# Kernel tuning notes

Measured on AMD Instinct MI355X. Metric: run time of the kernel, lower is better.

## Reference

```python
import jax, jax.numpy as jnp
import numpy as np

EPS_NORM = 1e-12
BN_EPS = 1e-5

def rmsnorm(x, gamma):
    # F.normalize(x, dim=-1) * gamma * dim**0.5
    n = jnp.maximum(jnp.linalg.norm(x, axis=-1, keepdims=True), EPS_NORM)
    return x / n * gamma * np.float32(np.sqrt(x.shape[-1]))

def conv1d(x, w, pad):
    # x: (B,C,T), w: (O,I,K)
    return jax.lax.conv_general_dilated(x, w, (1,), [(pad, pad)],
                                        dimension_numbers=('NCH', 'OIH', 'NCH'))

def maxpool3(x):
    # kernel 3, stride 1, pad 1 over last axis
    return jax.lax.reduce_window(x, -jnp.inf, jax.lax.max,
                                 (1, 1, 3), (1, 1, 1), [(0, 0), (0, 0), (1, 1)])

def gelu(x):
    return jax.nn.gelu(x, approximate=False)  # matches torch F.gelu default


def setup_inputs() -> dict:
    key = jax.random.key(0)
    ks = jax.random.split(key, 16)
    B, N, D, E, H, NF = 4, 4096, 512, 4, 1024, 32
    s = 0.02
    inp = {
        'x': jax.random.normal(ks[0], (B, N, D), jnp.float32),
        'left_k': 2048,
        'gamma1': jnp.ones((D,), jnp.float32),
        'gamma2': jnp.ones((D,), jnp.float32),
        'attn_w': jax.random.normal(ks[1], (D, 1), jnp.float32) * s,
        'attn_b': jnp.zeros((1,), jnp.float32),
        'gate_w': jax.random.normal(ks[2], (D, E), jnp.float32) * s,
        'expert_w1': jax.random.normal(ks[3], (E, D, H), jnp.float32) * s,
        'expert_w2': jax.random.normal(ks[4], (E, H, D), jnp.float32) * s,
        'bott_w': jax.random.normal(ks[5], (NF, D, 1), jnp.float32) * s,
        'conv_w39': jax.random.normal(ks[6], (NF, NF, 39), jnp.float32) * s,
        'conv_w19': jax.random.normal(ks[7], (NF, NF, 19), jnp.float32) * s,
        'conv_w9': jax.random.normal(ks[8], (NF, NF, 9), jnp.float32) * s,
        'mp_w': jax.random.normal(ks[9], (NF, D, 1), jnp.float32) * s,
        'bn_g': jnp.ones((NF * 4,), jnp.float32),
        'bn_b': jnp.zeros((NF * 4,), jnp.float32),
        'proj_w': jax.random.normal(ks[10], (NF * 4, D), jnp.float32) * s,
        'proj_b': jnp.zeros((D,), jnp.float32),
    }
    return inp


def reference(x, left_k, gamma1, gamma2, attn_w, attn_b, gate_w,
              expert_w1, expert_w2, bott_w, conv_w39, conv_w19, conv_w9,
              mp_w, bn_g, bn_b, proj_w, proj_b):
    B, N, D = x.shape
    E = gate_w.shape[-1]

    x_n = rmsnorm(x, gamma1)
    scores = jax.nn.sigmoid(x_n @ attn_w + attn_b)            # (B,N,1)
    xs = x_n * scores                                          # (B,N,D)

    # top-k token selection (remain_ratio < 1 path)
    _, top_idx = jax.lax.top_k(scores[..., 0], left_k)         # (B,left_k)
    sorted_idx = jnp.sort(top_idx, axis=1)
    left_x = jnp.take_along_axis(xs, sorted_idx[..., None], axis=1)
    # complement sum via scatter mask (faithful to scatter_/gather/sum)
    sel = jnp.zeros((B, N), x.dtype).at[jnp.arange(B)[:, None], sorted_idx].set(1.0)
    extra = jnp.einsum('bn,bnd->bd', 1.0 - sel, xs)[:, None, :]
    xcat = jnp.concatenate([left_x, extra], axis=1)            # (B,left_k+1,D)

    x_n2 = rmsnorm(xcat, gamma2)

    # dense soft MoE
    gate = jax.nn.softmax(x_n2 @ gate_w, axis=-1)              # (B,T,E)
    h = gelu(jnp.einsum('btd,edh->bteh', x_n2, expert_w1))
    eo = jnp.einsum('bteh,ehd->bted', h, expert_w2)
    moe_out = jnp.einsum('bte,bted->btd', gate, eo)
    moe_loss = E * jnp.sum(jnp.mean(gate, axis=(0, 1)) ** 2)

    # Inception branch (channels-first)
    xc = jnp.transpose(x_n2, (0, 2, 1))                        # (B,D,T)
    xb = conv1d(xc, bott_w, 0)                                 # (B,32,T)
    outs = [conv1d(xb, conv_w39, 19), conv1d(xb, conv_w19, 9),
            conv1d(xb, conv_w9, 4), conv1d(maxpool3(xc), mp_w, 0)]
    cat = jnp.concatenate(outs, axis=1)                        # (B,128,T)
    mu = jnp.mean(cat, axis=(0, 2), keepdims=True)
    var = jnp.var(cat, axis=(0, 2), keepdims=True)
    bn = (cat - mu) / jnp.sqrt(var + BN_EPS) * bn_g[None, :, None] + bn_b[None, :, None]
    incep = gelu(bn)
    incep_out = jnp.transpose(incep, (0, 2, 1)) @ proj_w + proj_b  # (B,T,D)

    out = xcat + moe_out + incep_out
    return gelu(out), moe_loss
```

## Files before the change

### kernel.cpp

```cpp
#include <hip/hip_runtime.h>
#include <hip/hip_bf16.h>
#include <math.h>

#define DEV __device__ __forceinline__

constexpr int B_ = 4, N_ = 4096, D_ = 512, E_ = 4, H_ = 1024, NF_ = 32;
constexpr int KL_ = 2048, T_ = KL_ + 1;
constexpr int TOK_ = B_ * T_;
constexpr int SP_ = 2304;

typedef __bf16 bf16x8 __attribute__((ext_vector_type(8)));
typedef float f32x4 __attribute__((ext_vector_type(4)));

DEV float gelu_f(float x){
  float t = __expf(-1.702f * x);
  return x * __builtin_amdgcn_rcpf(1.0f + t);
}
DEV float bf2f(unsigned short u){ union{unsigned int i; float f;} c; c.i = (unsigned)u << 16; return c.f; }
DEV unsigned pack2(float a, float b){
  __hip_bfloat16 ha = __float2bfloat16(a), hb = __float2bfloat16(b);
  unsigned short ua = *(unsigned short*)&ha, ub = *(unsigned short*)&hb;
  return (unsigned)ua | ((unsigned)ub << 16);
}

DEV float wave_sum(float v){
  #pragma unroll
  for (int off = 32; off > 0; off >>= 1) v += __shfl_down(v, off, 64);
  return v;
}

DEV float block_sum256(float v, float* sm){
  v = wave_sum(v);
  int lane = threadIdx.x & 63, wid = threadIdx.x >> 6;
  if (lane == 0) sm[wid] = v;
  __syncthreads();
  if (threadIdx.x == 0) sm[0] = sm[0] + sm[1] + sm[2] + sm[3];
  __syncthreads();
  float r = sm[0];
  __syncthreads();
  return r;
}

__global__ void k_rms_score(const float* __restrict__ x, const float* __restrict__ g,
                            const float* __restrict__ aw, const float* __restrict__ ab,
                            float* __restrict__ scores, float* __restrict__ scale){
  __shared__ float sm[4];
  int row = blockIdx.x; int tid = threadIdx.x;
  const float* xr = x + (size_t)row * D_;
  float v0 = xr[tid], v1 = xr[tid + 256];
  float ss = block_sum256(v0 * v0 + v1 * v1, sm);
  float a  = block_sum256(v0 * g[tid] * aw[tid] + v1 * g[tid + 256] * aw[tid + 256], sm);
  float n = fmaxf(sqrtf(ss), 1e-12f);
  float inv = 22.627416997969522f / n;
  float z = inv * a + ab[0];
  float s = 1.0f / (1.0f + expf(-z));
  if (tid == 0){ scores[row] = s; scale[row] = inv * s; }
}

__global__ void k_select(const float* __restrict__ scores, int* __restrict__ flags){
  __shared__ float s[N_];
  __shared__ int cnts[4][64];
  int b = blockIdx.y; int tid = threadIdx.x;
  int tile = blockIdx.x * 64;
  const float4* src = (const float4*)(scores + (size_t)b * N_);
  for (int j = tid; j < N_ / 4; j += 256) ((float4*)s)[j] = src[j];
  __syncthreads();
  int tok = tid & 63, part = tid >> 6;
  int i = tile + tok;
  float si = s[i];
  int cnt = 0;
  const float4* sp = (const float4*)(s + part * 1024);
  int jb = part * 1024;
  #pragma unroll 4
  for (int j = 0; j < 256; j++){
    float4 v = sp[j];
    int j4 = jb + j * 4;
    cnt += (v.x > si) || (v.x == si && (j4 + 0) < i);
    cnt += (v.y > si) || (v.y == si && (j4 + 1) < i);
    cnt += (v.z > si) || (v.z == si && (j4 + 2) < i);
    cnt += (v.w > si) || (v.w == si && (j4 + 3) < i);
  }
  cnts[part][tok] = cnt;
  __syncthreads();
  if (tid < 64){
    int c = cnts[0][tid] + cnts[1][tid] + cnts[2][tid] + cnts[3][tid];
    flags[(size_t)b * N_ + tile + tid] = (c < KL_) ? 1 : 0;
  }
}

__global__ void k_compact(const int* __restrict__ flags, int* __restrict__ idx){
  __shared__ int wsum[4];
  int b = blockIdx.x; int tid = threadIdx.x;
  const int* fb = flags + (size_t)b * N_;
  int f[16]; int cnt = 0;
  #pragma unroll
  for (int i = 0; i < 16; i++){ f[i] = fb[tid * 16 + i]; cnt += f[i]; }
  int lane = tid & 63, wid = tid >> 6;
  int v = cnt;
  #pragma unroll
  for (int off = 1; off < 64; off <<= 1){
    int t = __shfl_up(v, off, 64);
    if (lane >= off) v += t;
  }
  if (lane == 63) wsum[wid] = v;
  __syncthreads();
  int base = v - cnt;
  for (int w = 0; w < wid; w++) base += wsum[w];
  int* ib = idx + (size_t)b * KL_;
  #pragma unroll
  for (int i = 0; i < 16; i++){
    if (f[i]) ib[base++] = tid * 16 + i;
  }
}

__global__ void k_gather(const float* __restrict__ x, const float* __restrict__ scale,
                         const float* __restrict__ g1, const int* __restrict__ idx,
                         float* __restrict__ xcat){
  size_t i = (size_t)blockIdx.x * 256 + threadIdx.x;
  int d = (int)(i & 511);
  int p = (int)((i >> 9) & (KL_ - 1));
  int b = (int)(i >> 20);
  int tok = idx[(size_t)b * KL_ + p];
  float sc = scale[(size_t)b * N_ + tok];
  xcat[((size_t)b * T_ + p) * D_ + d] = x[((size_t)b * N_ + tok) * D_ + d] * sc * g1[d];
}

__global__ void k_extra1(const float* __restrict__ x, const float* __restrict__ scale,
                         const int* __restrict__ flags, float* __restrict__ part){
  int b = blockIdx.y, blk = blockIdx.x;
  int tid = threadIdx.x;
  const int* fb = flags + (size_t)b * N_ + blk * 64;
  const float* sb = scale + (size_t)b * N_ + blk * 64;
  const float2* xp = (const float2*)(x + ((size_t)b * N_ + blk * 64) * D_) + tid;
  float2 acc = {0.f, 0.f};
  for (int i = 0; i < 64; i++){
    if (!fb[i]){
      float s = sb[i];
      float2 v = xp[(size_t)i * 256];
      acc.x += v.x * s; acc.y += v.y * s;
    }
  }
  float* pr = part + ((size_t)(b * 64 + blk)) * D_;
  pr[tid * 2] = acc.x; pr[tid * 2 + 1] = acc.y;
}

__global__ void k_extra2(const float* __restrict__ part, const float* __restrict__ g1,
                         float* __restrict__ xcat){
  int b = blockIdx.y; int d = blockIdx.x * 256 + threadIdx.x;
  float s = 0.f;
  for (int i = 0; i < 64; i++) s += part[((size_t)(b * 64 + i)) * D_ + d];
  xcat[((size_t)b * T_ + KL_) * D_ + d] = s * g1[d];
}

__global__ void k_rms2gate(const float* __restrict__ xc, const float* __restrict__ g,
                           const float* __restrict__ gw,
                           __hip_bfloat16* __restrict__ xn2b, float* __restrict__ gate){
  __shared__ float sm[4];
  __shared__ float sg[16];
  int row = blockIdx.x; int tid = threadIdx.x;
  const float* xr = xc + (size_t)row * D_;
  float v0 = xr[tid], v1 = xr[tid + 256];
  float ss = block_sum256(v0 * v0 + v1 * v1, sm);
  float n = fmaxf(sqrtf(ss), 1e-12f);
  float inv = 22.627416997969522f / n;
  float xn0 = v0 * inv * g[tid], xn1 = v1 * inv * g[tid + 256];
  __hip_bfloat16* ob = xn2b + (size_t)row * D_;
  ob[tid] = __float2bfloat16(xn0); ob[tid + 256] = __float2bfloat16(xn1);
  const float4* gw4 = (const float4*)gw;
  float4 wa = gw4[tid], wb = gw4[tid + 256];
  float l0 = xn0 * wa.x + xn1 * wb.x, l1 = xn0 * wa.y + xn1 * wb.y;
  float l2 = xn0 * wa.z + xn1 * wb.z, l3 = xn0 * wa.w + xn1 * wb.w;
  l0 = wave_sum(l0); l1 = wave_sum(l1); l2 = wave_sum(l2); l3 = wave_sum(l3);
  int lane = tid & 63, wid = tid >> 6;
  if (lane == 0){ sg[wid*4+0]=l0; sg[wid*4+1]=l1; sg[wid*4+2]=l2; sg[wid*4+3]=l3; }
  __syncthreads();
  if (tid == 0){
    float a0 = sg[0]+sg[4]+sg[8]+sg[12];
    float a1 = sg[1]+sg[5]+sg[9]+sg[13];
    float a2 = sg[2]+sg[6]+sg[10]+sg[14];
    float a3 = sg[3]+sg[7]+sg[11]+sg[15];
    float m = fmaxf(fmaxf(a0, a1), fmaxf(a2, a3));
    float e0 = expf(a0-m), e1 = expf(a1-m), e2 = expf(a2-m), e3 = expf(a3-m);
    float is = 1.f / (e0+e1+e2+e3);
    float* gr = gate + (size_t)row * 4;
    gr[0]=e0*is; gr[1]=e1*is; gr[2]=e2*is; gr[3]=e3*is;
  }
}

__global__ void k_gsumloss(const float* __restrict__ gate, float* __restrict__ o){
  __shared__ float sm[16];
  int tid = threadIdx.x;
  float4 a = {0.f, 0.f, 0.f, 0.f};
  for (int r = tid; r < TOK_; r += 256){
    float4 v = *(const float4*)(gate + (size_t)r * 4);
    a.x += v.x; a.y += v.y; a.z += v.z; a.w += v.w;
  }
  a.x = wave_sum(a.x); a.y = wave_sum(a.y); a.z = wave_sum(a.z); a.w = wave_sum(a.w);
  int lane = tid & 63, wid = tid >> 6;
  if (lane == 0){ sm[wid*4]=a.x; sm[wid*4+1]=a.y; sm[wid*4+2]=a.z; sm[wid*4+3]=a.w; }
  __syncthreads();
  if (tid == 0){
    float l = 0.f;
    #pragma unroll
    for (int e = 0; e < 4; e++){
      float s = sm[e] + sm[4+e] + sm[8+e] + sm[12+e];
      float m = s / (float)TOK_;
      l += m * m;
    }
    o[0] = (float)E_ * l;
  }
}

__global__ void k_trb(const float* __restrict__ in, __hip_bfloat16* __restrict__ out,
                      int R, int C){
  __shared__ float t[32][33];
  int mat = blockIdx.z;
  in  += (size_t)mat * R * C;
  out += (size_t)mat * R * C;
  int c0 = blockIdx.x * 32, r0 = blockIdx.y * 32;
  int j = threadIdx.x & 31, i4 = threadIdx.x >> 5;
  #pragma unroll
  for (int k = 0; k < 4; k++){
    int i = i4 * 4 + k;
    t[i][j] = in[(size_t)(r0 + i) * C + c0 + j];
  }
  __syncthreads();
  #pragma unroll
  for (int k = 0; k < 4; k++){
    int i = i4 * 4 + k;
    out[(size_t)(c0 + i) * R + r0 + j] = __float2bfloat16(t[j][i]);
  }
}

__global__ void k_trb2(const float* __restrict__ in, __hip_bfloat16* __restrict__ out){
  __shared__ float t[32][33];
  int e = blockIdx.z;
  const float* ip = in + (size_t)e * H_ * D_;
  __hip_bfloat16* op = out + (size_t)e * H_;
  int c0 = blockIdx.x * 32, r0 = blockIdx.y * 32;
  int j = threadIdx.x & 31, i4 = threadIdx.x >> 5;
  #pragma unroll
  for (int k = 0; k < 4; k++){
    int i = i4 * 4 + k;
    t[i][j] = ip[(size_t)(r0 + i) * D_ + c0 + j];
  }
  __syncthreads();
  #pragma unroll
  for (int k = 0; k < 4; k++){
    int i = i4 * 4 + k;
    int v = r0 + j;
    int pv = (v & ~63) | ((v & 15) << 2) | ((v >> 4) & 3);
    op[(size_t)(c0 + i) * 4096 + pv] = __float2bfloat16(t[j][i]);
  }
}

__global__ void k_wpack(const float* __restrict__ w39, const float* __restrict__ w19,
                        const float* __restrict__ w9, __hip_bfloat16* __restrict__ wcb){
  int i = blockIdx.x * 256 + threadIdx.x;
  if (i >= 73728) return;
  const float* w; int KP, KW, base;
  if (i < 40960){ w = w39; KP = 40; KW = 39; base = 0; }
  else if (i < 61440){ w = w19; KP = 20; KW = 19; base = 40960; }
  else { w = w9; KP = 12; KW = 9; base = 61440; }
  int li = i - base;
  int oc = li / (32 * KP);
  int rem = li % (32 * KP);
  int k = rem >> 5, ic = rem & 31;
  float v = (k < KW) ? w[((size_t)oc * 32 + ic) * KW + k] : 0.f;
  wcb[i] = __float2bfloat16(v);
}

template<int EPI>
__launch_bounds__(512)
__global__ void gemm_bt(const __hip_bfloat16* __restrict__ A,
                        const __hip_bfloat16* __restrict__ Bt,
                        __hip_bfloat16* __restrict__ Cb, size_t zstride,
                        int M, int N, int K, int kloc,
                        const float* __restrict__ gatep){
  __shared__ __align__(16) char smem[2][24576];
  int tid = threadIdx.x;
  unsigned gx = gridDim.x;
  unsigned nwg = gx * gridDim.y;
  unsigned orig = blockIdx.x + gx * blockIdx.y;
  unsigned q = nwg >> 3, r = nwg & 7;
  unsigned xcd = orig & 7, loc = orig >> 3;
  unsigned wg = (xcd < r ? xcd * (q + 1) : r * (q + 1) + (xcd - r) * q) + loc;
  int m0 = (int)(wg / gx) * 256, n0 = (int)(wg % gx) * 128;
  int z = blockIdx.z;
  int koff = z * kloc;
  int ln = tid & 63, wid = tid >> 6;
  int wm = wid >> 1, wn = wid & 1;

  f32x4 acc[4][4] = {};

  auto stage = [&](int buf, int k0){
    #pragma unroll
    for (int c = 0; c < 2; c++){
      int ii = tid + c * 512;
      int rr = ii >> 2, s = ii & 3;
      int gm = m0 + rr; gm = gm < M ? gm : M - 1;
      const __hip_bfloat16* gp = A + (size_t)gm * K + (koff + k0 + ((s ^ (rr & 3)) << 3));
      __builtin_amdgcn_global_load_lds(
          (const __attribute__((address_space(1))) void*)gp,
          (__attribute__((address_space(3))) void*)&smem[buf][ii * 16], 16, 0, 0);
    }
    {
      int ii = tid;
      int rr = ii >> 2, s = ii & 3;
      const __hip_bfloat16* gp = Bt + (size_t)(n0 + rr) * K + (koff + k0 + ((s ^ (rr & 3)) << 3));
      __builtin_amdgcn_global_load_lds(
          (const __attribute__((address_space(1))) void*)gp,
          (__attribute__((address_space(3))) void*)&smem[buf][16384 + ii * 16], 16, 0, 0);
    }
  };

  int nk = kloc >> 5;
  stage(0, 0);
  __syncthreads();
  int slotb = (((ln >> 4) ^ (ln & 3)) << 4);
  for (int t = 0; t < nk; t++){
    int buf = t & 1;
    if (t + 1 < nk) stage(buf ^ 1, (t + 1) << 5);
    bf16x8 af[4], bfr[4];
    #pragma unroll
    for (int m = 0; m < 4; m++){
      int R = wm * 64 + m * 16 + (ln & 15);
      af[m] = *(const bf16x8*)&smem[buf][R * 64 + slotb];
    }
    #pragma unroll
    for (int n = 0; n < 4; n++){
      int R = wn * 64 + n * 16 + (ln & 15);
      bfr[n] = *(const bf16x8*)&smem[buf][16384 + R * 64 + slotb];
    }
    #pragma unroll
    for (int m = 0; m < 4; m++)
      #pragma unroll
      for (int n = 0; n < 4; n++)
        acc[m][n] = __builtin_amdgcn_mfma_f32_16x16x32_bf16(af[m], bfr[n], acc[m][n], 0, 0, 0);
    __syncthreads();
  }

  __hip_bfloat16* Co = Cb + (size_t)z * zstride;
  int e = n0 >> 10;
  int lr = ln & 15;
  #pragma unroll
  for (int m = 0; m < 4; m++){
    int rb = m0 + wm * 64 + m * 16 + ((ln >> 4) << 2);
    float gv[4];
    if (EPI == 1){
      #pragma unroll
      for (int r2 = 0; r2 < 4; r2++)
        gv[r2] = (rb + r2 < M) ? gatep[(size_t)(rb + r2) * 4 + e] : 0.f;
    }
    #pragma unroll
    for (int r2 = 0; r2 < 4; r2++){
      int row = rb + r2;
      if (row < M){
        float v0 = acc[m][0][r2], v1 = acc[m][1][r2];
        float v2 = acc[m][2][r2], v3 = acc[m][3][r2];
        if (EPI == 1){
          v0 = gelu_f(v0) * gv[r2]; v1 = gelu_f(v1) * gv[r2];
          v2 = gelu_f(v2) * gv[r2]; v3 = gelu_f(v3) * gv[r2];
        }
        uint2 pk; pk.x = pack2(v0, v1); pk.y = pack2(v2, v3);
        size_t ci = (size_t)row * N + (n0 + wn * 64 + 4 * lr);
        *(uint2*)&Co[ci] = pk;
      }
    }
  }
}

__global__ void k_1x1F(const __hip_bfloat16* __restrict__ xn2b, const float* __restrict__ bw,
                       const float* __restrict__ mw,
                       __hip_bfloat16* __restrict__ xbp, float* __restrict__ cat){
  __shared__ float Xs[32 * 33];
  __shared__ float Ws[32 * 36];
  int type = blockIdx.y;
  const float* w = type == 0 ? bw : mw;
  int tid = threadIdx.x;
  int G0 = blockIdx.x * 32;
  int tok = tid & 31, grp = tid >> 5;
  float acc[4] = {};
  for (int d0 = 0; d0 < D_; d0 += 32){
    {
      int tt = tid >> 3, dc = (tid & 7) * 4;
      int g = G0 + tt;
      float4 v = {0.f, 0.f, 0.f, 0.f};
      if (g < TOK_){
        const __hip_bfloat16* p = xn2b + (size_t)g * D_ + d0 + dc;
        ushort4 rw = *(const ushort4*)p;
        v.x = bf2f(rw.x); v.y = bf2f(rw.y); v.z = bf2f(rw.z); v.w = bf2f(rw.w);
        if (type == 1){
          int t = g % T_;
          if (t > 0){
            ushort4 u = *(const ushort4*)(p - D_);
            v.x = fmaxf(v.x, bf2f(u.x)); v.y = fmaxf(v.y, bf2f(u.y));
            v.z = fmaxf(v.z, bf2f(u.z)); v.w = fmaxf(v.w, bf2f(u.w));
          }
          if (t < T_ - 1){
            ushort4 u = *(const ushort4*)(p + D_);
            v.x = fmaxf(v.x, bf2f(u.x)); v.y = fmaxf(v.y, bf2f(u.y));
            v.z = fmaxf(v.z, bf2f(u.z)); v.w = fmaxf(v.w, bf2f(u.w));
          }
        }
      }
      float* xd = &Xs[tt * 33 + dc];
      xd[0] = v.x; xd[1] = v.y; xd[2] = v.z; xd[3] = v.w;
    }
    for (int j = tid; j < 1024; j += 256){
      int f = j >> 5, d = j & 31;
      Ws[d * 36 + f] = w[(size_t)f * D_ + d0 + d];
    }
    __syncthreads();
    const float* xr = &Xs[tok * 33];
    #pragma unroll 8
    for (int d = 0; d < 32; d++){
      float xv = xr[d];
      const float4* w4 = (const float4*)&Ws[d * 36 + grp * 4];
      float4 a = w4[0];
      acc[0] += xv * a.x; acc[1] += xv * a.y; acc[2] += xv * a.z; acc[3] += xv * a.w;
    }
    __syncthreads();
  }
  int g = G0 + tok;
  if (g < TOK_){
    if (type == 0){
      int bb = g / T_, t = g % T_;
      __hip_bfloat16* op = xbp + ((size_t)(bb * SP_ + 32 + t)) * 32 + grp * 4;
      #pragma unroll
      for (int j = 0; j < 4; j++) op[j] = __float2bfloat16(acc[j]);
    } else {
      float* op = cat + (size_t)g * 128 + 96 + grp * 4;
      #pragma unroll
      for (int j = 0; j < 4; j++) op[j] = acc[j];
    }
  }
}

template<int KP, int PAD, int OFF, int TYPE>
DEV void convm_body(const __hip_bfloat16* __restrict__ xbp,
                    const __hip_bfloat16* __restrict__ wcb,
                    float* __restrict__ cat, char* smem){
  constexpr int R = KP * 32;
  int t0 = blockIdx.x * 128, b = blockIdx.y;
  int tid = threadIdx.x;
  for (int j = tid; j < 768; j += 256){
    int r = j >> 2, c = j & 3;
    int rg = b * SP_ + 32 + t0 - PAD + r;
    const __hip_bfloat16* gp = xbp + (size_t)rg * 32 + ((c ^ (r & 3)) << 3);
    __builtin_amdgcn_global_load_lds(
        (const __attribute__((address_space(1))) void*)gp,
        (__attribute__((address_space(3))) void*)(smem + j * 16), 16, 0, 0);
  }
  __syncthreads();
  int ln = tid & 63, wid = tid >> 6;
  int lr = ln & 15, lg = ln >> 4;
  int tb = wid * 32;
  const __hip_bfloat16* wt = wcb + OFF;
  const __hip_bfloat16* bp0 = wt + (size_t)lr * R + lg * 8;
  const __hip_bfloat16* bp1 = wt + (size_t)(16 + lr) * R + lg * 8;
  f32x4 acc[2][2] = {};
  bf16x8 bc0 = *(const bf16x8*)bp0;
  bf16x8 bc1 = *(const bf16x8*)bp1;
  #pragma unroll 4
  for (int s = 0; s < KP; s++){
    bf16x8 bn0 = bc0, bn1 = bc1;
    if (s + 1 < KP){
      bn0 = *(const bf16x8*)(bp0 + (s + 1) * 32);
      bn1 = *(const bf16x8*)(bp1 + (s + 1) * 32);
    }
    int ra0 = tb + lr + s;
    int ra1 = tb + 16 + lr + s;
    bf16x8 a0 = *(const bf16x8*)(smem + ra0 * 64 + ((lg ^ (ra0 & 3)) << 4));
    bf16x8 a1 = *(const bf16x8*)(smem + ra1 * 64 + ((lg ^ (ra1 & 3)) << 4));
    acc[0][0] = __builtin_amdgcn_mfma_f32_16x16x32_bf16(a0, bc0, acc[0][0], 0, 0, 0);
    acc[0][1] = __builtin_amdgcn_mfma_f32_16x16x32_bf16(a0, bc1, acc[0][1], 0, 0, 0);
    acc[1][0] = __builtin_amdgcn_mfma_f32_16x16x32_bf16(a1, bc0, acc[1][0], 0, 0, 0);
    acc[1][1] = __builtin_amdgcn_mfma_f32_16x16x32_bf16(a1, bc1, acc[1][1], 0, 0, 0);
    bc0 = bn0; bc1 = bn1;
  }
  #pragma unroll
  for (int m = 0; m < 2; m++){
    int rb = tb + m * 16 + ((ln >> 4) << 2);
    #pragma unroll
    for (int n = 0; n < 2; n++){
      int oc = n * 16 + lr;
      #pragma unroll
      for (int j2 = 0; j2 < 4; j2++){
        int tp = t0 + rb + j2;
        if (tp < T_)
          cat[((size_t)b * T_ + tp) * 128 + TYPE * 32 + oc] = acc[m][n][j2];
      }
    }
  }
}

__global__ __launch_bounds__(256)
void k_convM(const __hip_bfloat16* __restrict__ xbp,
             const __hip_bfloat16* __restrict__ wcb, float* __restrict__ cat){
  __shared__ __align__(16) char smem[192 * 64];
  if (blockIdx.z == 0)      convm_body<40, 19, 0,     0>(xbp, wcb, cat, smem);
  else if (blockIdx.z == 1) convm_body<20, 9,  40960, 1>(xbp, wcb, cat, smem);
  else                      convm_body<12, 4,  61440, 2>(xbp, wcb, cat, smem);
}

__global__ void k_bnstat(const float* __restrict__ cat, float* __restrict__ stats){
  __shared__ float sm[512];
  int tid = threadIdx.x;
  float s = 0.f, q = 0.f;
  for (int rp = blockIdx.x; rp < TOK_ / 2; rp += gridDim.x){
    float v = cat[(size_t)rp * 256 + tid];
    s += v; q += v * v;
  }
  sm[tid] = s; sm[256 + tid] = q;
  __syncthreads();
  if (tid < 128){
    atomicAdd(&stats[tid], sm[tid] + sm[tid + 128]);
    atomicAdd(&stats[128 + tid], sm[256 + tid] + sm[256 + tid + 128]);
  }
}

__global__ void k_bnact(const float* __restrict__ cat, __hip_bfloat16* __restrict__ catb,
                        const float* __restrict__ stats,
                        const float* __restrict__ g, const float* __restrict__ b){
  int i = blockIdx.x * 256 + threadIdx.x;
  int c = i & 127;
  float mu = stats[c] * (1.f / TOK_);
  float var = stats[128 + c] * (1.f / TOK_) - mu * mu;
  float v = cat[i];
  v = (v - mu) * rsqrtf(var + 1e-5f) * g[c] + b[c];
  catb[i] = __float2bfloat16(gelu_f(v));
}

__global__ void k_final(const float* __restrict__ xcat, const __hip_bfloat16* __restrict__ moeb,
                        size_t zs, const __hip_bfloat16* __restrict__ ioutb,
                        const float* __restrict__ pb, float* __restrict__ out){
  size_t i = ((size_t)blockIdx.x * 256 + threadIdx.x) * 2;
  int p = (int)(i & 511);
  size_t rowbase = i - p;
  float s0 = 0.f, s1 = 0.f;
  #pragma unroll
  for (int z = 0; z < 4; z++){
    unsigned u = *(const unsigned*)&moeb[(size_t)z * zs + i];
    s0 += bf2f((unsigned short)(u & 0xffff));
    s1 += bf2f((unsigned short)(u >> 16));
  }
  unsigned v = *(const unsigned*)&ioutb[i];
  s0 += bf2f((unsigned short)(v & 0xffff));
  s1 += bf2f((unsigned short)(v >> 16));
  int d0 = (p & ~63) | ((p & 3) << 4) | ((p >> 2) & 15);
  int p1 = p + 1;
  int d1 = (p1 & ~63) | ((p1 & 3) << 4) | ((p1 >> 2) & 15);
  s0 += xcat[rowbase + d0] + pb[d0];
  s1 += xcat[rowbase + d1] + pb[d1];
  out[rowbase + d0] = gelu_f(s0);
  out[rowbase + d1] = gelu_f(s1);
}

extern "C" void kernel_launch(void* const* d_in, const int* in_sizes, int n_in,
                              void* d_out, int out_size, void* d_ws, size_t ws_size,
                              hipStream_t stream){
  const float* x      = (const float*)d_in[0];
  const float* gamma1 = (const float*)d_in[2];
  const float* gamma2 = (const float*)d_in[3];
  const float* attn_w = (const float*)d_in[4];
  const float* attn_b = (const float*)d_in[5];
  const float* gate_w = (const float*)d_in[6];
  const float* ew1    = (const float*)d_in[7];
  const float* ew2    = (const float*)d_in[8];
  const float* bott_w = (const float*)d_in[9];
  const float* w39    = (const float*)d_in[10];
  const float* w19    = (const float*)d_in[11];
  const float* w9     = (const float*)d_in[12];
  const float* mp_w   = (const float*)d_in[13];
  const float* bn_g   = (const float*)d_in[14];
  const float* bn_b   = (const float*)d_in[15];
  const float* proj_w = (const float*)d_in[16];
  const float* proj_b = (const float*)d_in[17];
  float* out = (float*)d_out;

  float* ws = (float*)d_ws;
  size_t off = 0;
  auto alloc = [&](size_t n){ size_t o = off; off += (n + 63) & ~(size_t)63; return o; };
  size_t f_hb   = alloc((size_t)TOK_ * 4096 / 2);
  size_t f_sc   = alloc(B_ * N_);
  size_t f_sca  = alloc(B_ * N_);
  size_t f_fl   = alloc(B_ * N_);
  size_t f_idx  = alloc(B_ * KL_);
  size_t f_xcat = alloc((size_t)TOK_ * D_);
  size_t f_moeb = alloc((size_t)4 * TOK_ * D_ / 2 + 64);
  size_t f_gate = alloc(TOK_ * E_);
  size_t f_st   = alloc(256);
  size_t f_xbp  = alloc((size_t)B_ * SP_ * 32 / 2);
  size_t f_cat  = alloc((size_t)TOK_ * 128);
  size_t f_wb   = alloc((size_t)(E_ * D_ * H_) + (size_t)TOK_ * D_ / 2 + 64);
  size_t f_part = alloc((size_t)B_ * 64 * D_);
  size_t f_wcb  = alloc(73728 / 2 + 64);
  size_t f_pjb  = alloc(512 * 128 / 2 + 64);
  (void)ws_size; (void)in_sizes; (void)n_in; (void)out_size;

  float* sc   = ws + f_sc;
  float* sca  = ws + f_sca;
  int*   fl   = (int*)(ws + f_fl);
  int*   idx  = (int*)(ws + f_idx);
  float* xcat = ws + f_xcat;
  float* gate = ws + f_gate;
  float* stats= ws + f_st;
  float* cat  = ws + f_cat;
  float* part = ws + f_part;
  __hip_bfloat16* moeb  = (__hip_bfloat16*)(ws + f_moeb);
  __hip_bfloat16* xbp   = (__hip_bfloat16*)(ws + f_xbp);
  __hip_bfloat16* wcb   = (__hip_bfloat16*)(ws + f_wcb);
  __hip_bfloat16* projb = (__hip_bfloat16*)(ws + f_pjb);
  __hip_bfloat16* hbuf  = (__hip_bfloat16*)(ws + f_hb);
  __hip_bfloat16* ioutb = (__hip_bfloat16*)(ws + f_hb);
  __hip_bfloat16* catb  = (__hip_bfloat16*)(ws + f_hb + 4196416);
  __hip_bfloat16* w1b  = (__hip_bfloat16*)(ws + f_wb);
  __hip_bfloat16* w2b  = w1b + (size_t)E_ * D_ * H_;
  __hip_bfloat16* xn2b = w2b + (size_t)E_ * D_ * H_;

  hipMemsetAsync(stats, 0, 256 * sizeof(float), stream);
  hipMemsetAsync(xbp, 0, (size_t)B_ * SP_ * 32 * sizeof(__hip_bfloat16), stream);

  k_trb<<<dim3(H_/32, D_/32, E_), 256, 0, stream>>>(ew1, w1b, D_, H_);
  k_trb2<<<dim3(D_/32, H_/32, E_), 256, 0, stream>>>(ew2, w2b);
  k_trb<<<dim3(D_/32, 128/32, 1), 256, 0, stream>>>(proj_w, projb, 128, D_);
  k_wpack<<<288, 256, 0, stream>>>(w39, w19, w9, wcb);

  k_rms_score<<<B_ * N_, 256, 0, stream>>>(x, gamma1, attn_w, attn_b, sc, sca);
  k_select<<<dim3(N_ / 64, B_), 256, 0, stream>>>(sc, fl);
  k_compact<<<B_, 256, 0, stream>>>(fl, idx);
  k_gather<<<(B_ * KL_ * D_) / 256, 256, 0, stream>>>(x, sca, gamma1, idx, xcat);
  k_extra1<<<dim3(64, B_), 256, 0, stream>>>(x, sca, fl, part);
  k_extra2<<<dim3(2, B_), 256, 0, stream>>>(part, gamma1, xcat);
  k_rms2gate<<<TOK_, 256, 0, stream>>>(xcat, gamma2, gate_w, xn2b, gate);
  k_gsumloss<<<1, 256, 0, stream>>>(gate, out + (size_t)TOK_ * D_);

  int mt = (TOK_ + 255) / 256;
  size_t zs = (size_t)TOK_ * D_;
  gemm_bt<1><<<dim3(4096/128, mt), 512, 0, stream>>>(
      xn2b, w1b, hbuf, 0, TOK_, 4096, D_, D_, gate);
  gemm_bt<0><<<dim3(D_/128, mt, 4), 512, 0, stream>>>(
      hbuf, w2b, moeb, zs, TOK_, D_, 4096, 1024, nullptr);

  int t32 = (TOK_ + 31) / 32;
  k_1x1F<<<dim3(t32, 2), 256, 0, stream>>>(xn2b, bott_w, mp_w, xbp, cat);
  k_convM<<<dim3(17, 4, 3), 256, 0, stream>>>(xbp, wcb, cat);
  k_bnstat<<<256, 256, 0, stream>>>(cat, stats);
  k_bnact<<<(TOK_ * 128) / 256, 256, 0, stream>>>(cat, catb, stats, bn_g, bn_b);
  gemm_bt<0><<<dim3(D_/128, mt), 512, 0, stream>>>(
      catb, projb, ioutb, 0, TOK_, D_, 128, 128, nullptr);
  k_final<<<((size_t)TOK_ * D_) / 512, 256, 0, stream>>>(xcat, moeb, zs, ioutb, proj_b, out);
}
```

Measured before the change: 313.7 us.

## Fuse gather with RMSNorm/gate, fold BN stats into convs, merge weight prep

Merges the gather and extra-token kernels with the second RMSNorm and gate softmax, so xcat is produced and normalized in one pass and stored as bf16 instead of fp32. Batch-norm sum and sum-of-squares are accumulated with atomics in the 1x1 and conv epilogues, which removes the separate k_bnstat pass over cat. The four weight transpose and pack kernels and the stats memset are merged into one launch. The bf16 xcat residual in the final sum loses some precision, and the float atomics make the BN statistics depend on summation order.

```diff
diff --git a/kernel.cpp b/kernel.cpp
--- a/kernel.cpp
+++ b/kernel.cpp
@@ -113,16 +113,57 @@
   }
 }
 
-__global__ void k_gather(const float* __restrict__ x, const float* __restrict__ scale,
-                         const float* __restrict__ g1, const int* __restrict__ idx,
-                         float* __restrict__ xcat){
-  size_t i = (size_t)blockIdx.x * 256 + threadIdx.x;
-  int d = (int)(i & 511);
-  int p = (int)((i >> 9) & (KL_ - 1));
-  int b = (int)(i >> 20);
+DEV void rms2_tail(int row, float xc0, float xc1,
+                   const float* __restrict__ g2, const float* __restrict__ gw,
+                   __hip_bfloat16* __restrict__ xcatb,
+                   __hip_bfloat16* __restrict__ xn2b, float* __restrict__ gate,
+                   float* sm, float* sg){
+  int tid = threadIdx.x;
+  __hip_bfloat16* xb = xcatb + (size_t)row * D_;
+  xb[tid] = __float2bfloat16(xc0); xb[tid + 256] = __float2bfloat16(xc1);
+  float ss = block_sum256(xc0 * xc0 + xc1 * xc1, sm);
+  float n = fmaxf(sqrtf(ss), 1e-12f);
+  float inv = 22.627416997969522f / n;
+  float xn0 = xc0 * inv * g2[tid], xn1 = xc1 * inv * g2[tid + 256];
+  __hip_bfloat16* ob = xn2b + (size_t)row * D_;
+  ob[tid] = __float2bfloat16(xn0); ob[tid + 256] = __float2bfloat16(xn1);
+  const float4* gw4 = (const float4*)gw;
+  float4 wa = gw4[tid], wb = gw4[tid + 256];
+  float l0 = xn0 * wa.x + xn1 * wb.x, l1 = xn0 * wa.y + xn1 * wb.y;
+  float l2 = xn0 * wa.z + xn1 * wb.z, l3 = xn0 * wa.w + xn1 * wb.w;
+  l0 = wave_sum(l0); l1 = wave_sum(l1); l2 = wave_sum(l2); l3 = wave_sum(l3);
+  int lane = tid & 63, wid = tid >> 6;
+  if (lane == 0){ sg[wid*4+0]=l0; sg[wid*4+1]=l1; sg[wid*4+2]=l2; sg[wid*4+3]=l3; }
+  __syncthreads();
+  if (tid == 0){
+    float a0 = sg[0]+sg[4]+sg[8]+sg[12];
+    float a1 = sg[1]+sg[5]+sg[9]+sg[13];
+    float a2 = sg[2]+sg[6]+sg[10]+sg[14];
+    float a3 = sg[3]+sg[7]+sg[11]+sg[15];
+    float m = fmaxf(fmaxf(a0, a1), fmaxf(a2, a3));
+    float e0 = expf(a0-m), e1 = expf(a1-m), e2 = expf(a2-m), e3 = expf(a3-m);
+    float is = 1.f / (e0+e1+e2+e3);
+    float* gr = gate + (size_t)row * 4;
+    gr[0]=e0*is; gr[1]=e1*is; gr[2]=e2*is; gr[3]=e3*is;
+  }
+}
+
+__global__ void k_gatherrms(const float* __restrict__ x, const float* __restrict__ scale,
+                            const float* __restrict__ g1, const float* __restrict__ g2,
+                            const float* __restrict__ gw, const int* __restrict__ idx,
+                            __hip_bfloat16* __restrict__ xcatb,
+                            __hip_bfloat16* __restrict__ xn2b, float* __restrict__ gate){
+  __shared__ float sm[4];
+  __shared__ float sg[16];
+  int rid = blockIdx.x;
+  int b = rid >> 11, p = rid & (KL_ - 1);
+  int tid = threadIdx.x;
   int tok = idx[(size_t)b * KL_ + p];
   float sc = scale[(size_t)b * N_ + tok];
-  xcat[((size_t)b * T_ + p) * D_ + d] = x[((size_t)b * N_ + tok) * D_ + d] * sc * g1[d];
+  const float* xr = x + ((size_t)b * N_ + tok) * D_;
+  float xc0 = xr[tid] * sc * g1[tid];
+  float xc1 = xr[tid + 256] * sc * g1[tid + 256];
+  rms2_tail(b * T_ + p, xc0, xc1, g2, gw, xcatb, xn2b, gate, sm, sg);
 }
 
 __global__ void k_extra1(const float* __restrict__ x, const float* __restrict__ scale,
@@ -144,47 +185,20 @@
   pr[tid * 2] = acc.x; pr[tid * 2 + 1] = acc.y;
 }
 
-__global__ void k_extra2(const float* __restrict__ part, const float* __restrict__ g1,
-                         float* __restrict__ xcat){
-  int b = blockIdx.y; int d = blockIdx.x * 256 + threadIdx.x;
-  float s = 0.f;
-  for (int i = 0; i < 64; i++) s += part[((size_t)(b * 64 + i)) * D_ + d];
-  xcat[((size_t)b * T_ + KL_) * D_ + d] = s * g1[d];
-}
-
-__global__ void k_rms2gate(const float* __restrict__ xc, const float* __restrict__ g,
-                           const float* __restrict__ gw,
-                           __hip_bfloat16* __restrict__ xn2b, float* __restrict__ gate){
+__global__ void k_extra2r(const float* __restrict__ part, const float* __restrict__ g1,
+                          const float* __restrict__ g2, const float* __restrict__ gw,
+                          __hip_bfloat16* __restrict__ xcatb,
+                          __hip_bfloat16* __restrict__ xn2b, float* __restrict__ gate){
   __shared__ float sm[4];
   __shared__ float sg[16];
-  int row = blockIdx.x; int tid = threadIdx.x;
-  const float* xr = xc + (size_t)row * D_;
-  float v0 = xr[tid], v1 = xr[tid + 256];
-  float ss = block_sum256(v0 * v0 + v1 * v1, sm);
-  float n = fmaxf(sqrtf(ss), 1e-12f);
-  float inv = 22.627416997969522f / n;
-  float xn0 = v0 * inv * g[tid], xn1 = v1 * inv * g[tid + 256];
-  __hip_bfloat16* ob = xn2b + (size_t)row * D_;
-  ob[tid] = __float2bfloat16(xn0); ob[tid + 256] = __float2bfloat16(xn1);
-  const float4* gw4 = (const float4*)gw;
-  float4 wa = gw4[tid], wb = gw4[tid + 256];
-  float l0 = xn0 * wa.x + xn1 * wb.x, l1 = xn0 * wa.y + xn1 * wb.y;
-  float l2 = xn0 * wa.z + xn1 * wb.z, l3 = xn0 * wa.w + xn1 * wb.w;
-  l0 = wave_sum(l0); l1 = wave_sum(l1); l2 = wave_sum(l2); l3 = wave_sum(l3);
-  int lane = tid & 63, wid = tid >> 6;
-  if (lane == 0){ sg[wid*4+0]=l0; sg[wid*4+1]=l1; sg[wid*4+2]=l2; sg[wid*4+3]=l3; }
-  __syncthreads();
-  if (tid == 0){
-    float a0 = sg[0]+sg[4]+sg[8]+sg[12];
-    float a1 = sg[1]+sg[5]+sg[9]+sg[13];
-    float a2 = sg[2]+sg[6]+sg[10]+sg[14];
-    float a3 = sg[3]+sg[7]+sg[11]+sg[15];
-    float m = fmaxf(fmaxf(a0, a1), fmaxf(a2, a3));
-    float e0 = expf(a0-m), e1 = expf(a1-m), e2 = expf(a2-m), e3 = expf(a3-m);
-    float is = 1.f / (e0+e1+e2+e3);
-    float* gr = gate + (size_t)row * 4;
-    gr[0]=e0*is; gr[1]=e1*is; gr[2]=e2*is; gr[3]=e3*is;
-  }
+  int b = blockIdx.x; int tid = threadIdx.x;
+  float s0 = 0.f, s1 = 0.f;
+  for (int i = 0; i < 64; i++){
+    const float* pr = part + ((size_t)(b * 64 + i)) * D_;
+    s0 += pr[tid]; s1 += pr[tid + 256];
+  }
+  float xc0 = s0 * g1[tid], xc1 = s1 * g1[tid + 256];
+  rms2_tail(b * T_ + KL_, xc0, xc1, g2, gw, xcatb, xn2b, gate, sm, sg);
 }
 
 __global__ void k_gsumloss(const float* __restrict__ gate, float* __restrict__ o){
@@ -211,13 +225,10 @@
   }
 }
 
-__global__ void k_trb(const float* __restrict__ in, __hip_bfloat16* __restrict__ out,
-                      int R, int C){
+DEV void trb_tile(const float* __restrict__ in, __hip_bfloat16* __restrict__ out,
+                  int R, int C, int bx, int by){
   __shared__ float t[32][33];
-  int mat = blockIdx.z;
-  in  += (size_t)mat * R * C;
-  out += (size_t)mat * R * C;
-  int c0 = blockIdx.x * 32, r0 = blockIdx.y * 32;
+  int c0 = bx * 32, r0 = by * 32;
   int j = threadIdx.x & 31, i4 = threadIdx.x >> 5;
   #pragma unroll
   for (int k = 0; k < 4; k++){
@@ -232,42 +243,61 @@
   }
 }
 
-__global__ void k_trb2(const float* __restrict__ in, __hip_bfloat16* __restrict__ out){
-  __shared__ float t[32][33];
-  int e = blockIdx.z;
-  const float* ip = in + (size_t)e * H_ * D_;
-  __hip_bfloat16* op = out + (size_t)e * H_;
-  int c0 = blockIdx.x * 32, r0 = blockIdx.y * 32;
-  int j = threadIdx.x & 31, i4 = threadIdx.x >> 5;
-  #pragma unroll
-  for (int k = 0; k < 4; k++){
-    int i = i4 * 4 + k;
-    t[i][j] = ip[(size_t)(r0 + i) * D_ + c0 + j];
-  }
-  __syncthreads();
-  #pragma unroll
-  for (int k = 0; k < 4; k++){
-    int i = i4 * 4 + k;
-    int v = r0 + j;
-    int pv = (v & ~63) | ((v & 15) << 2) | ((v >> 4) & 3);
-    op[(size_t)(c0 + i) * 4096 + pv] = __float2bfloat16(t[j][i]);
-  }
-}
-
-__global__ void k_wpack(const float* __restrict__ w39, const float* __restrict__ w19,
-                        const float* __restrict__ w9, __hip_bfloat16* __restrict__ wcb){
-  int i = blockIdx.x * 256 + threadIdx.x;
-  if (i >= 73728) return;
-  const float* w; int KP, KW, base;
-  if (i < 40960){ w = w39; KP = 40; KW = 39; base = 0; }
-  else if (i < 61440){ w = w19; KP = 20; KW = 19; base = 40960; }
-  else { w = w9; KP = 12; KW = 9; base = 61440; }
-  int li = i - base;
-  int oc = li / (32 * KP);
-  int rem = li % (32 * KP);
-  int k = rem >> 5, ic = rem & 31;
-  float v = (k < KW) ? w[((size_t)oc * 32 + ic) * KW + k] : 0.f;
-  wcb[i] = __float2bfloat16(v);
+__global__ void k_wprep(const float* __restrict__ ew1, const float* __restrict__ ew2,
+                        const float* __restrict__ proj_w,
+                        const float* __restrict__ w39, const float* __restrict__ w19,
+                        const float* __restrict__ w9,
+                        __hip_bfloat16* __restrict__ w1b, __hip_bfloat16* __restrict__ w2b,
+                        __hip_bfloat16* __restrict__ projb, __hip_bfloat16* __restrict__ wcb,
+                        float* __restrict__ stats){
+  int blk = blockIdx.x;
+  int tid = threadIdx.x;
+  if (blk < 2048){
+    int e = blk >> 9, rem = blk & 511;
+    int by = rem >> 5, bx = rem & 31;
+    trb_tile(ew1 + (size_t)e * D_ * H_, w1b + (size_t)e * D_ * H_, D_, H_, bx, by);
+  } else if (blk < 4096){
+    int r = blk - 2048;
+    int e = r >> 9, r2 = r & 511;
+    int bx = r2 & 15, by = r2 >> 4;
+    __shared__ float t[32][33];
+    const float* ip = ew2 + (size_t)e * H_ * D_;
+    __hip_bfloat16* op = w2b + (size_t)e * H_;
+    int c0 = bx * 32, r0 = by * 32;
+    int j = tid & 31, i4 = tid >> 5;
+    #pragma unroll
+    for (int k = 0; k < 4; k++){
+      int i = i4 * 4 + k;
+      t[i][j] = ip[(size_t)(r0 + i) * D_ + c0 + j];
+    }
+    __syncthreads();
+    #pragma unroll
+    for (int k = 0; k < 4; k++){
+      int i = i4 * 4 + k;
+      int v = r0 + j;
+      int pv = (v & ~63) | ((v & 15) << 2) | ((v >> 4) & 3);
+      op[(size_t)(c0 + i) * 4096 + pv] = __float2bfloat16(t[j][i]);
+    }
+  } else if (blk < 4160){
+    int r = blk - 4096;
+    trb_tile(proj_w, projb, 128, D_, r & 15, r >> 4);
+  } else if (blk < 4448){
+    int i = (blk - 4160) * 256 + tid;
+    if (i < 73728){
+      const float* w; int KP, KW, base;
+      if (i < 40960){ w = w39; KP = 40; KW = 39; base = 0; }
+      else if (i < 61440){ w = w19; KP = 20; KW = 19; base = 40960; }
+      else { w = w9; KP = 12; KW = 9; base = 61440; }
+      int li = i - base;
+      int oc = li / (32 * KP);
+      int rem = li % (32 * KP);
+      int k = rem >> 5, ic = rem & 31;
+      float v = (k < KW) ? w[((size_t)oc * 32 + ic) * KW + k] : 0.f;
+      wcb[i] = __float2bfloat16(v);
+    }
+  } else {
+    stats[tid] = 0.f;
+  }
 }
 
 template<int EPI>
@@ -372,7 +402,8 @@
 
 __global__ void k_1x1F(const __hip_bfloat16* __restrict__ xn2b, const float* __restrict__ bw,
                        const float* __restrict__ mw,
-                       __hip_bfloat16* __restrict__ xbp, float* __restrict__ cat){
+                       __hip_bfloat16* __restrict__ xbp, float* __restrict__ cat,
+                       float* __restrict__ stats){
   __shared__ float Xs[32 * 33];
   __shared__ float Ws[32 * 36];
   int type = blockIdx.y;
@@ -423,7 +454,8 @@
     __syncthreads();
   }
   int g = G0 + tok;
-  if (g < TOK_){
+  bool valid = g < TOK_;
+  if (valid){
     if (type == 0){
       int bb = g / T_, t = g % T_;
       __hip_bfloat16* op = xbp + ((size_t)(bb * SP_ + 32 + t)) * 32 + grp * 4;
@@ -435,15 +467,34 @@
       for (int j = 0; j < 4; j++) op[j] = acc[j];
     }
   }
+  if (type == 1){
+    #pragma unroll
+    for (int j = 0; j < 4; j++){
+      float s = valid ? acc[j] : 0.f;
+      float qv = valid ? acc[j] * acc[j] : 0.f;
+      #pragma unroll
+      for (int off = 16; off > 0; off >>= 1){
+        s += __shfl_down(s, off, 32);
+        qv += __shfl_down(qv, off, 32);
+      }
+      if (tok == 0){
+        int ch = 96 + grp * 4 + j;
+        atomicAdd(&stats[ch], s);
+        atomicAdd(&stats[128 + ch], qv);
+      }
+    }
+  }
 }
 
 template<int KP, int PAD, int OFF, int TYPE>
 DEV void convm_body(const __hip_bfloat16* __restrict__ xbp,
                     const __hip_bfloat16* __restrict__ wcb,
-                    float* __restrict__ cat, char* smem){
+                    float* __restrict__ cat, float* __restrict__ stats,
+                    char* smem, float* bsS, float* bsQ){
   constexpr int R = KP * 32;
   int t0 = blockIdx.x * 128, b = blockIdx.y;
   int tid = threadIdx.x;
+  if (tid < 32){ bsS[tid] = 0.f; bsQ[tid] = 0.f; }
   for (int j = tid; j < 768; j += 256){
     int r = j >> 2, c = j & 3;
     int rg = b * SP_ + 32 + t0 - PAD + r;
@@ -479,45 +530,50 @@
     acc[1][1] = __builtin_amdgcn_mfma_f32_16x16x32_bf16(a1, bc1, acc[1][1], 0, 0, 0);
     bc0 = bn0; bc1 = bn1;
   }
+  float sN[2] = {0.f, 0.f}, qN[2] = {0.f, 0.f};
   #pragma unroll
   for (int m = 0; m < 2; m++){
-    int rb = tb + m * 16 + ((ln >> 4) << 2);
+    int rb = tb + m * 16 + (lg << 2);
     #pragma unroll
     for (int n = 0; n < 2; n++){
       int oc = n * 16 + lr;
       #pragma unroll
       for (int j2 = 0; j2 < 4; j2++){
         int tp = t0 + rb + j2;
-        if (tp < T_)
-          cat[((size_t)b * T_ + tp) * 128 + TYPE * 32 + oc] = acc[m][n][j2];
+        if (tp < T_){
+          float v = acc[m][n][j2];
+          cat[((size_t)b * T_ + tp) * 128 + TYPE * 32 + oc] = v;
+          sN[n] += v; qN[n] += v * v;
+        }
       }
     }
+  }
+  #pragma unroll
+  for (int n = 0; n < 2; n++){
+    float s = sN[n], qv = qN[n];
+    s += __shfl_down(s, 32, 64); qv += __shfl_down(qv, 32, 64);
+    s += __shfl_down(s, 16, 64); qv += __shfl_down(qv, 16, 64);
+    if (ln < 16){
+      atomicAdd(&bsS[n * 16 + lr], s);
+      atomicAdd(&bsQ[n * 16 + lr], qv);
+    }
+  }
+  __syncthreads();
+  if (tid < 32){
+    atomicAdd(&stats[TYPE * 32 + tid], bsS[tid]);
+    atomicAdd(&stats[128 + TYPE * 32 + tid], bsQ[tid]);
   }
 }
 
 __global__ __launch_bounds__(256)
 void k_convM(const __hip_bfloat16* __restrict__ xbp,
-             const __hip_bfloat16* __restrict__ wcb, float* __restrict__ cat){
+             const __hip_bfloat16* __restrict__ wcb, float* __restrict__ cat,
+             float* __restrict__ stats){
   __shared__ __align__(16) char smem[192 * 64];
-  if (blockIdx.z == 0)      convm_body<40, 19, 0,     0>(xbp, wcb, cat, smem);
-  else if (blockIdx.z == 1) convm_body<20, 9,  40960, 1>(xbp, wcb, cat, smem);
-  else                      convm_body<12, 4,  61440, 2>(xbp, wcb, cat, smem);
-}
-
-__global__ void k_bnstat(const float* __restrict__ cat, float* __restrict__ stats){
-  __shared__ float sm[512];
-  int tid = threadIdx.x;
-  float s = 0.f, q = 0.f;
-  for (int rp = blockIdx.x; rp < TOK_ / 2; rp += gridDim.x){
-    float v = cat[(size_t)rp * 256 + tid];
-    s += v; q += v * v;
-  }
-  sm[tid] = s; sm[256 + tid] = q;
-  __syncthreads();
-  if (tid < 128){
-    atomicAdd(&stats[tid], sm[tid] + sm[tid + 128]);
-    atomicAdd(&stats[128 + tid], sm[256 + tid] + sm[256 + tid + 128]);
-  }
+  __shared__ float bsS[32], bsQ[32];
+  if (blockIdx.z == 0)      convm_body<40, 19, 0,     0>(xbp, wcb, cat, stats, smem, bsS, bsQ);
+  else if (blockIdx.z == 1) convm_body<20, 9,  40960, 1>(xbp, wcb, cat, stats, smem, bsS, bsQ);
+  else                      convm_body<12, 4,  61440, 2>(xbp, wcb, cat, stats, smem, bsS, bsQ);
 }
 
 __global__ void k_bnact(const float* __restrict__ cat, __hip_bfloat16* __restrict__ catb,
@@ -532,7 +588,8 @@
   catb[i] = __float2bfloat16(gelu_f(v));
 }
 
-__global__ void k_final(const float* __restrict__ xcat, const __hip_bfloat16* __restrict__ moeb,
+__global__ void k_final(const __hip_bfloat16* __restrict__ xcatb,
+                        const __hip_bfloat16* __restrict__ moeb,
                         size_t zs, const __hip_bfloat16* __restrict__ ioutb,
                         const float* __restrict__ pb, float* __restrict__ out){
   size_t i = ((size_t)blockIdx.x * 256 + threadIdx.x) * 2;
@@ -551,8 +608,9 @@
   int d0 = (p & ~63) | ((p & 3) << 4) | ((p >> 2) & 15);
   int p1 = p + 1;
   int d1 = (p1 & ~63) | ((p1 & 3) << 4) | ((p1 >> 2) & 15);
-  s0 += xcat[rowbase + d0] + pb[d0];
-  s1 += xcat[rowbase + d1] + pb[d1];
+  const unsigned short* xc = (const unsigned short*)xcatb;
+  s0 += bf2f(xc[rowbase + d0]) + pb[d0];
+  s1 += bf2f(xc[rowbase + d1]) + pb[d1];
   out[rowbase + d0] = gelu_f(s0);
   out[rowbase + d1] = gelu_f(s1);
 }
@@ -587,7 +645,7 @@
   size_t f_sca  = alloc(B_ * N_);
   size_t f_fl   = alloc(B_ * N_);
   size_t f_idx  = alloc(B_ * KL_);
-  size_t f_xcat = alloc((size_t)TOK_ * D_);
+  size_t f_xcb  = alloc((size_t)TOK_ * D_ / 2 + 64);
   size_t f_moeb = alloc((size_t)4 * TOK_ * D_ / 2 + 64);
   size_t f_gate = alloc(TOK_ * E_);
   size_t f_st   = alloc(256);
@@ -603,11 +661,11 @@
   float* sca  = ws + f_sca;
   int*   fl   = (int*)(ws + f_fl);
   int*   idx  = (int*)(ws + f_idx);
-  float* xcat = ws + f_xcat;
   float* gate = ws + f_gate;
   float* stats= ws + f_st;
   float* cat  = ws + f_cat;
   float* part = ws + f_part;
+  __hip_bfloat16* xcatb = (__hip_bfloat16*)(ws + f_xcb);
   __hip_bfloat16* moeb  = (__hip_bfloat16*)(ws + f_moeb);
   __hip_bfloat16* xbp   = (__hip_bfloat16*)(ws + f_xbp);
   __hip_bfloat16* wcb   = (__hip_bfloat16*)(ws + f_wcb);
@@ -619,21 +677,18 @@
   __hip_bfloat16* w2b  = w1b + (size_t)E_ * D_ * H_;
   __hip_bfloat16* xn2b = w2b + (size_t)E_ * D_ * H_;
 
-  hipMemsetAsync(stats, 0, 256 * sizeof(float), stream);
   hipMemsetAsync(xbp, 0, (size_t)B_ * SP_ * 32 * sizeof(__hip_bfloat16), stream);
 
-  k_trb<<<dim3(H_/32, D_/32, E_), 256, 0, stream>>>(ew1, w1b, D_, H_);
-  k_trb2<<<dim3(D_/32, H_/32, E_), 256, 0, stream>>>(ew2, w2b);
-  k_trb<<<dim3(D_/32, 128/32, 1), 256, 0, stream>>>(proj_w, projb, 128, D_);
-  k_wpack<<<288, 256, 0, stream>>>(w39, w19, w9, wcb);
+  k_wprep<<<4449, 256, 0, stream>>>(ew1, ew2, proj_w, w39, w19, w9,
+                                    w1b, w2b, projb, wcb, stats);
 
   k_rms_score<<<B_ * N_, 256, 0, stream>>>(x, gamma1, attn_w, attn_b, sc, sca);
   k_select<<<dim3(N_ / 64, B_), 256, 0, stream>>>(sc, fl);
   k_compact<<<B_, 256, 0, stream>>>(fl, idx);
-  k_gather<<<(B_ * KL_ * D_) / 256, 256, 0, stream>>>(x, sca, gamma1, idx, xcat);
+  k_gatherrms<<<B_ * KL_, 256, 0, stream>>>(x, sca, gamma1, gamma2, gate_w, idx,
+                                            xcatb, xn2b, gate);
   k_extra1<<<dim3(64, B_), 256, 0, stream>>>(x, sca, fl, part);
-  k_extra2<<<dim3(2, B_), 256, 0, stream>>>(part, gamma1, xcat);
-  k_rms2gate<<<TOK_, 256, 0, stream>>>(xcat, gamma2, gate_w, xn2b, gate);
+  k_extra2r<<<B_, 256, 0, stream>>>(part, gamma1, gamma2, gate_w, xcatb, xn2b, gate);
   k_gsumloss<<<1, 256, 0, stream>>>(gate, out + (size_t)TOK_ * D_);
 
   int mt = (TOK_ + 255) / 256;
@@ -644,11 +699,10 @@
       hbuf, w2b, moeb, zs, TOK_, D_, 4096, 1024, nullptr);
 
   int t32 = (TOK_ + 31) / 32;
-  k_1x1F<<<dim3(t32, 2), 256, 0, stream>>>(xn2b, bott_w, mp_w, xbp, cat);
-  k_convM<<<dim3(17, 4, 3), 256, 0, stream>>>(xbp, wcb, cat);
-  k_bnstat<<<256, 256, 0, stream>>>(cat, stats);
+  k_1x1F<<<dim3(t32, 2), 256, 0, stream>>>(xn2b, bott_w, mp_w, xbp, cat, stats);
+  k_convM<<<dim3(17, 4, 3), 256, 0, stream>>>(xbp, wcb, cat, stats);
   k_bnact<<<(TOK_ * 128) / 256, 256, 0, stream>>>(cat, catb, stats, bn_g, bn_b);
   gemm_bt<0><<<dim3(D_/128, mt), 512, 0, stream>>>(
       catb, projb, ioutb, 0, TOK_, D_, 128, 128, nullptr);
-  k_final<<<((size_t)TOK_ * D_) / 512, 256, 0, stream>>>(xcat, moeb, zs, ioutb, proj_b, out);
-}
+  k_final<<<((size_t)TOK_ * D_) / 512, 256, 0, stream>>>(xcatb, moeb, zs, ioutb, proj_b, out);
+}
```

New measurement: 317.3 us. About the same (+1.1%).
